# Optimization experiments

Hardware: AMD Instinct MI355X
Metric: run time of the kernel (lower is better)

Reference implementation:

```python
import jax, jax.numpy as jnp
from jax import lax
import numpy as np

NUM_CLASSES = 10
NUM_ITERS = 3


def conv2d(x, w, stride):
    return lax.conv_general_dilated(x, w, window_strides=stride, padding='VALID',
                                    dimension_numbers=('NCHW', 'OIHW', 'NCHW'))


def deconv(x, w_torch, stride, pad):
    # w_torch: [Cin, Cout, k, k] (PyTorch ConvTranspose2d layout)
    k = w_torch.shape[2]
    w = jnp.flip(w_torch, axis=(2, 3)).transpose(1, 0, 2, 3)  # -> [Cout, Cin, k, k]
    return lax.conv_general_dilated(x, w, window_strides=(1, 1),
                                    padding=[(k - 1 - pad, k - 1 - pad)] * 2,
                                    lhs_dilation=(stride, stride),
                                    dimension_numbers=('NCHW', 'OIHW', 'NCHW'))


def squash(t, axis=-1):
    sq = jnp.sum(t * t, axis=axis, keepdims=True)
    return (sq / (1.0 + sq)) * t / jnp.sqrt(sq)


def batchnorm(t, g, b, eps=1e-5):
    # training-mode batch statistics over (N, H, W)
    m = t.mean(axis=(0, 2, 3), keepdims=True)
    v = t.var(axis=(0, 2, 3), keepdims=True)
    return g[None, :, None, None] * (t - m) / jnp.sqrt(v + eps) + b[None, :, None, None]


def setup_inputs() -> dict:
    key = jax.random.key(0)
    ks = jax.random.split(key, 16)
    B = 128
    d = dict(
        x=jax.random.normal(ks[0], (B, 3, 32, 32), jnp.float32),
        conv1_w=jax.random.normal(ks[1], (256, 3, 9, 9), jnp.float32) * 0.05,
        conv1_b=jnp.zeros((256,), jnp.float32),
        prim_w=jax.random.normal(ks[2], (8, 64, 256, 9, 9), jnp.float32) * 0.02,
        prim_b=jnp.zeros((8, 64), jnp.float32),
        route_w=jax.random.normal(ks[3], (NUM_CLASSES, 4096, 8, 16), jnp.float32),
        g1_w=jax.random.normal(ks[4], (160, 256, 4, 4), jnp.float32) * 0.02,
        g2_w=jax.random.normal(ks[5], (256, 128, 4, 4), jnp.float32) * 0.02,
        g3_w=jax.random.normal(ks[6], (128, 64, 4, 4), jnp.float32) * 0.02,
        g4_w=jax.random.normal(ks[7], (64, 3, 4, 4), jnp.float32) * 0.02,
        bn1_g=jnp.ones((256,), jnp.float32), bn1_b=jnp.zeros((256,), jnp.float32),
        bn2_g=jnp.ones((128,), jnp.float32), bn2_b=jnp.zeros((128,), jnp.float32),
        bn3_g=jnp.ones((64,), jnp.float32), bn3_b=jnp.zeros((64,), jnp.float32),
    )
    return d


def reference(x, conv1_w, conv1_b, prim_w, prim_b, route_w,
              g1_w, g2_w, g3_w, g4_w,
              bn1_g, bn1_b, bn2_g, bn2_b, bn3_g, bn3_b):
    B = x.shape[0]
    # conv stem: [B,3,32,32] -> [B,256,24,24]
    h = jax.nn.relu(conv2d(x, conv1_w, (1, 1)) + conv1_b[None, :, None, None])
    # primary capsules: 8 parallel convs fused into one [8*64,256,9,9] conv -> [B,512,8,8]
    u = conv2d(h, prim_w.reshape(8 * 64, 256, 9, 9), (2, 2)) + prim_b.reshape(8 * 64)[None, :, None, None]
    # cat over capsules on last dim: route node = flat (c,h,w) per capsule -> [B,4096,8]
    u = u.reshape(B, 8, 64 * 8 * 8).transpose(0, 2, 1)
    u = squash(u, axis=-1)
    # digit capsules: priors [C,B,R,16]
    priors = jnp.einsum('bri,crio->cbro', u, route_w)
    logits = jnp.zeros(priors.shape[:3], priors.dtype)  # [C,B,R]
    v = None
    for i in range(NUM_ITERS):
        probs = jax.nn.softmax(logits, axis=2)  # over route nodes (dim=2 in original)
        v = squash(jnp.einsum('cbr,cbro->cbo', probs, priors), axis=-1)  # [C,B,16]
        if i != NUM_ITERS - 1:
            logits = logits + jnp.einsum('cbro,cbo->cbr', priors, v)
    caps = v.transpose(1, 0, 2)  # [B,10,16]
    classes = jax.nn.softmax(jnp.sqrt(jnp.sum(caps * caps, axis=-1)), axis=-1)  # [B,10]
    # y = one-hot of predicted class (inference path, y=None)
    y = jax.nn.one_hot(jnp.argmax(classes, axis=1), NUM_CLASSES, dtype=caps.dtype)
    z = (caps * y[:, :, None]).reshape(B, 160, 1, 1)
    # DCGAN generator: 1 -> 4 -> 8 -> 16 -> 32
    t = jax.nn.relu(batchnorm(deconv(z, g1_w, 1, 0), bn1_g, bn1_b))
    t = jax.nn.relu(batchnorm(deconv(t, g2_w, 2, 1), bn2_g, bn2_b))
    t = jax.nn.relu(batchnorm(deconv(t, g3_w, 2, 1), bn3_g, bn3_b))
    recon = jnp.tanh(deconv(t, g4_w, 2, 1))  # [B,3,32,32]
    return classes, recon
```

## Files before the change

### kernel.cpp

```cpp
#include <hip/hip_runtime.h>
#include <cmath>

#define NB 128

#define H_STRIDE 600
#define W_SLAB   7776

__global__ __launch_bounds__(192) void conv1_kernel(
    const float* __restrict__ x, const float* __restrict__ w,
    const float* __restrict__ bias, float* __restrict__ h)
{
    __shared__ float4 xs4[768];
    float* xs = (float*)xs4;
    int b = blockIdx.x, cobase = blockIdx.y * 8, tid = threadIdx.x;
    const float4* xsrc = (const float4*)(x + (size_t)b * 3072);
    for (int i = tid; i < 768; i += 192) xs4[i] = xsrc[i];
    __syncthreads();
    for (int round = 0; round < 3; ++round) {
        int px = round * 192 + tid;
        int yy = px / 24, xx = px - yy * 24;
        float acc[8];
        #pragma unroll
        for (int cc = 0; cc < 8; ++cc) acc[cc] = 0.f;
        for (int c = 0; c < 3; ++c)
            for (int ky = 0; ky < 9; ++ky) {
                const float* xr = xs + c * 1024 + (yy + ky) * 32 + xx;
                float xv[9];
                #pragma unroll
                for (int kx = 0; kx < 9; ++kx) xv[kx] = xr[kx];
                int tb = c * 81 + ky * 9;
                #pragma unroll
                for (int cc = 0; cc < 8; ++cc) {
                    const float* wp = w + (cobase + cc) * 243 + tb;
                    #pragma unroll
                    for (int kx = 0; kx < 9; ++kx) acc[cc] += xv[kx] * wp[kx];
                }
            }
        #pragma unroll
        for (int cc = 0; cc < 8; ++cc)
            h[((size_t)b * 256 + cobase + cc) * H_STRIDE + yy * 25 + xx] =
                fmaxf(acc[cc] + bias[cobase + cc], 0.f);
    }
}

__global__ __launch_bounds__(128) void primw_transpose_kernel(
    const float* __restrict__ pw, float* __restrict__ wt)
{
    int g = blockIdx.x >> 8, ci = blockIdx.x & 255;
    int half = threadIdx.x >> 6, lane = threadIdx.x & 63;
    for (int ch = half; ch < 64; ch += 2) {
        int oct = ch >> 3, k = ch & 7;
        const float* src = pw + ((size_t)(g * 64 + ch) * 256 + ci) * 81;
        float* dst = wt + (size_t)(g * 256 + ci) * W_SLAB + oct * 12 + k;
        dst[(size_t)lane * 96] = src[lane];
        if (lane < 17) dst[(size_t)(64 + lane) * 96] = src[64 + lane];
    }
}

__global__ __launch_bounds__(128) void prim_conv_kernel(
    const float* __restrict__ h, const float* __restrict__ wt,
    float* __restrict__ part)
{
    __shared__ __align__(16) float wsh[W_SLAB];
    __shared__ __align__(16) float hsh[H_STRIDE];
    int b = blockIdx.x, g = blockIdx.y, half = blockIdx.z, tid = threadIdx.x;
    int ci0 = half * 128;
    int oct = tid & 7;
    int pq = tid >> 3;
    int px0 = pq * 4;
    int y0 = pq >> 1, x0 = (pq & 1) * 4;

    float acc[8][4];
    #pragma unroll
    for (int i = 0; i < 8; ++i)
        #pragma unroll
        for (int j = 0; j < 4; ++j) acc[i][j] = 0.f;

    #define STAGE(ci)                                                                        \
    {                                                                                        \
        const float* wsrc = wt + (size_t)(g * 256 + (ci)) * W_SLAB;                          \
        const float* hsrc = h + ((size_t)b * 256 + (ci)) * H_STRIDE;                         \
        _Pragma("unroll")                                                                    \
        for (int k = 0; k < 16; ++k) {                                                       \
            int ix = k * 128 + tid;                                                          \
            if (ix < 1944)                                                                   \
                __builtin_amdgcn_global_load_lds(                                            \
                    (const unsigned int*)wsrc + ix * 4,                                      \
                    (unsigned int*)wsh + ix * 4, 16, 0, 0);                                  \
        }                                                                                    \
        __builtin_amdgcn_global_load_lds(                                                    \
            (const unsigned int*)hsrc + tid * 4,                                             \
            (unsigned int*)hsh + tid * 4, 16, 0, 0);                                         \
        if (tid < 22)                                                                        \
            __builtin_amdgcn_global_load_lds(                                                \
                (const unsigned int*)hsrc + (128 + tid) * 4,                                 \
                (unsigned int*)hsh + (128 + tid) * 4, 16, 0, 0);                             \
    }

    STAGE(ci0);
    asm volatile("s_waitcnt vmcnt(0)" ::: "memory");
    __syncthreads();

    for (int ci = ci0; ci < ci0 + 128; ++ci) {
        #pragma unroll 3
        for (int ky = 0; ky < 9; ++ky) {
            int hrowbase = (2 * y0 + ky) * 25 + 2 * x0;
            #pragma unroll
            for (int kx = 0; kx < 9; ++kx) {
                const float* wp = wsh + (ky * 9 + kx) * 96 + oct * 12;
                float4 wa = *(const float4*)(wp);
                float4 wb = *(const float4*)(wp + 4);
                int hr = hrowbase + kx;
                float h0 = hsh[hr];
                float h1 = hsh[hr + 2];
                float h2 = hsh[hr + 4];
                float h3 = hsh[hr + 6];
                float wv[8] = {wa.x, wa.y, wa.z, wa.w, wb.x, wb.y, wb.z, wb.w};
                #pragma unroll
                for (int i = 0; i < 8; ++i) {
                    acc[i][0] += wv[i] * h0;
                    acc[i][1] += wv[i] * h1;
                    acc[i][2] += wv[i] * h2;
                    acc[i][3] += wv[i] * h3;
                }
            }
        }
        __syncthreads();
        if (ci + 1 < ci0 + 128) STAGE(ci + 1);
        asm volatile("s_waitcnt vmcnt(0)" ::: "memory");
        __syncthreads();
    }
    #undef STAGE

    float* pp = part + ((size_t)(half * 128 + b) * 8 + g) * 4096;
    #pragma unroll
    for (int i = 0; i < 8; ++i) {
        int c64 = oct * 8 + i;
        *(float4*)(pp + c64 * 64 + px0) =
            make_float4(acc[i][0], acc[i][1], acc[i][2], acc[i][3]);
    }
}

__global__ void squash_u_kernel(const float* __restrict__ part,
                                const float* __restrict__ pb, float* __restrict__ ut)
{
    int b = blockIdx.x; int r = blockIdx.y * 256 + threadIdx.x;
    int c64 = r >> 6;
    const float* p0 = part + (size_t)b * 8 * 4096 + r;
    const float* p1 = part + (size_t)(128 + b) * 8 * 4096 + r;
    float v[8]; float sq = 0.f;
    #pragma unroll
    for (int i = 0; i < 8; ++i) {
        v[i] = p0[(size_t)i * 4096] + p1[(size_t)i * 4096] + pb[i * 64 + c64];
        sq += v[i] * v[i];
    }
    float sc = sqrtf(sq) / (1.f + sq);
    float4 o0 = make_float4(v[0] * sc, v[1] * sc, v[2] * sc, v[3] * sc);
    float4 o1 = make_float4(v[4] * sc, v[5] * sc, v[6] * sc, v[7] * sc);
    float* o = ut + ((size_t)b * 4096 + r) * 8;
    *(float4*)o = o0; *(float4*)(o + 4) = o1;
}

__global__ void softmax_stats_kernel(const float* __restrict__ logits,
                                     float* __restrict__ mbuf, float* __restrict__ sebuf)
{
    int cb = blockIdx.x; int tid = threadIdx.x;
    const float* lrow = logits + (size_t)cb * 4096;
    float mx = -1e30f;
    for (int i = tid; i < 4096; i += 256) mx = fmaxf(mx, lrow[i]);
    #pragma unroll
    for (int d = 1; d < 64; d <<= 1) mx = fmaxf(mx, __shfl_xor(mx, d));
    __shared__ float rm[4], rs[4];
    if ((tid & 63) == 0) rm[tid >> 6] = mx;
    __syncthreads();
    mx = fmaxf(fmaxf(rm[0], rm[1]), fmaxf(rm[2], rm[3]));
    float s = 0.f;
    for (int i = tid; i < 4096; i += 256) s += expf(lrow[i] - mx);
    #pragma unroll
    for (int d = 1; d < 64; d <<= 1) s += __shfl_xor(s, d);
    if ((tid & 63) == 0) rs[tid >> 6] = s;
    __syncthreads();
    if (tid == 0) {
        mbuf[cb] = mx;
        sebuf[cb] = rs[0] + rs[1] + rs[2] + rs[3];
    }
}

__global__ __launch_bounds__(256) void route_s_kernel(
    const float* __restrict__ logits, const float* __restrict__ ut,
    const float* __restrict__ route_w, const float* __restrict__ mbuf,
    const float* __restrict__ sebuf, float* __restrict__ spart)
{
    __shared__ __align__(16) float smem[11232];
    const int UB = 4224, PB = 8400, RB = 8928;
    int c = blockIdx.x, ch = blockIdx.y, tid = threadIdx.x;
    int r0 = ch * 32;

    {
        const float4* w4 = (const float4*)(route_w + ((size_t)c * 4096 + r0) * 128);
        #pragma unroll
        for (int k = 0; k < 4; ++k) {
            int idx = k * 256 + tid;
            float4 wv = w4[idx];
            int rl = idx >> 5, rem = (idx & 31) * 4;
            *(float4*)(smem + rl * 132 + rem) = wv;
        }
    }

    int bC = tid & 15, igC = (tid >> 4) & 7, ohC = tid >> 7;

    for (int bg = 0; bg < 8; ++bg) {
        int b0 = bg * 16;
        __syncthreads();
        {
            int bb = tid >> 4, seg = tid & 15;
            const float4* us = (const float4*)(ut + (size_t)(b0 + bb) * 32768 + (size_t)r0 * 8);
            #pragma unroll
            for (int q = 0; q < 4; ++q) {
                float4 v = us[seg * 4 + q];
                int base = UB + bb * 261 + (seg * 4 + q) * 4;
                smem[base + 0] = v.x; smem[base + 1] = v.y;
                smem[base + 2] = v.z; smem[base + 3] = v.w;
            }
        }
        if (tid < 128) {
            int b = tid >> 3, rr = tid & 7;
            int cb = c * 128 + b0 + b;
            float m = mbuf[cb];
            float inv = 1.0f / sebuf[cb];
            float4 lv = *(const float4*)(logits + (size_t)cb * 4096 + r0 + rr * 4);
            int pbb = PB + b * 33 + rr * 4;
            smem[pbb + 0] = expf(lv.x - m) * inv;
            smem[pbb + 1] = expf(lv.y - m) * inv;
            smem[pbb + 2] = expf(lv.z - m) * inv;
            smem[pbb + 3] = expf(lv.w - m) * inv;
        }
        __syncthreads();
        float4 a0 = make_float4(0.f, 0.f, 0.f, 0.f);
        float4 a1 = make_float4(0.f, 0.f, 0.f, 0.f);
        int ub = UB + bC * 261 + igC;
        int wb = igC * 16 + ohC * 8;
        int pbb = PB + bC * 33;
        for (int rl = 0; rl < 32; ++rl) {
            float uu = smem[ub + rl * 8];
            float pr = smem[pbb + rl];
            float t1 = pr * uu;
            const float* wp = smem + rl * 132 + wb;
            float4 w0 = *(const float4*)wp;
            float4 w1 = *(const float4*)(wp + 4);
            a0.x += t1 * w0.x; a0.y += t1 * w0.y; a0.z += t1 * w0.z; a0.w += t1 * w0.w;
            a1.x += t1 * w1.x; a1.y += t1 * w1.y; a1.z += t1 * w1.z; a1.w += t1 * w1.w;
        }
        int rb = RB + tid * 9;
        smem[rb + 0] = a0.x; smem[rb + 1] = a0.y; smem[rb + 2] = a0.z; smem[rb + 3] = a0.w;
        smem[rb + 4] = a1.x; smem[rb + 5] = a1.y; smem[rb + 6] = a1.z; smem[rb + 7] = a1.w;
        __syncthreads();
        {
            int o = tid & 15, b = tid >> 4;
            int oh = o >> 3, ol = o & 7;
            float s = 0.f;
            #pragma unroll
            for (int ig = 0; ig < 8; ++ig)
                s += smem[RB + (b + 16 * ig + 128 * oh) * 9 + ol];
            spart[(size_t)ch * 20480 + (size_t)(c * 128 + b0 + b) * 16 + o] = s;
        }
    }
}

__global__ void route_v_kernel(const float* __restrict__ spart, float* __restrict__ vbuf)
{
    int cb = blockIdx.x * 64 + threadIdx.x;
    float4 a0 = make_float4(0,0,0,0), a1 = make_float4(0,0,0,0);
    float4 a2 = make_float4(0,0,0,0), a3 = make_float4(0,0,0,0);
    for (int k = 0; k < 128; ++k) {
        const float4* p = (const float4*)(spart + (size_t)k * 20480 + (size_t)cb * 16);
        float4 b0 = p[0], b1 = p[1], b2 = p[2], b3 = p[3];
        a0.x += b0.x; a0.y += b0.y; a0.z += b0.z; a0.w += b0.w;
        a1.x += b1.x; a1.y += b1.y; a1.z += b1.z; a1.w += b1.w;
        a2.x += b2.x; a2.y += b2.y; a2.z += b2.z; a2.w += b2.w;
        a3.x += b3.x; a3.y += b3.y; a3.z += b3.z; a3.w += b3.w;
    }
    float sq = a0.x*a0.x + a0.y*a0.y + a0.z*a0.z + a0.w*a0.w
             + a1.x*a1.x + a1.y*a1.y + a1.z*a1.z + a1.w*a1.w
             + a2.x*a2.x + a2.y*a2.y + a2.z*a2.z + a2.w*a2.w
             + a3.x*a3.x + a3.y*a3.y + a3.z*a3.z + a3.w*a3.w;
    float sc = sqrtf(sq) / (1.f + sq);
    float4* vp = (float4*)(vbuf + (size_t)cb * 16);
    vp[0] = make_float4(a0.x*sc, a0.y*sc, a0.z*sc, a0.w*sc);
    vp[1] = make_float4(a1.x*sc, a1.y*sc, a1.z*sc, a1.w*sc);
    vp[2] = make_float4(a2.x*sc, a2.y*sc, a2.z*sc, a2.w*sc);
    vp[3] = make_float4(a3.x*sc, a3.y*sc, a3.z*sc, a3.w*sc);
}

__global__ __launch_bounds__(256) void route_upd_kernel(
    float* __restrict__ logits, const float* __restrict__ ut,
    const float* __restrict__ route_w, const float* __restrict__ vbuf)
{
    __shared__ __align__(16) float smem[8400];
    const int UB = 4224;
    int c = blockIdx.x, ch = blockIdx.y, tid = threadIdx.x;
    int r0 = ch * 32;
    {
        const float4* w4 = (const float4*)(route_w + ((size_t)c * 4096 + r0) * 128);
        #pragma unroll
        for (int k = 0; k < 4; ++k) {
            int idx = k * 256 + tid;
            float4 wv = w4[idx];
            int rl = idx >> 5, rem = (idx & 31) * 4;
            *(float4*)(smem + rl * 132 + rem) = wv;
        }
    }
    int b = tid & 15, rg = tid >> 4;
    for (int bg = 0; bg < 8; ++bg) {
        int b0 = bg * 16;
        __syncthreads();
        {
            int bb = tid >> 4, seg = tid & 15;
            const float4* us = (const float4*)(ut + (size_t)(b0 + bb) * 32768 + (size_t)r0 * 8);
            #pragma unroll
            for (int q = 0; q < 4; ++q) {
                float4 v = us[seg * 4 + q];
                int base = UB + bb * 261 + (seg * 4 + q) * 4;
                smem[base + 0] = v.x; smem[base + 1] = v.y;
                smem[base + 2] = v.z; smem[base + 3] = v.w;
            }
        }
        __syncthreads();
        int cb = c * 128 + b0 + b;
        const float4* vp = (const float4*)(vbuf + (size_t)cb * 16);
        float4 v0 = vp[0], v1 = vp[1], v2 = vp[2], v3 = vp[3];
        #pragma unroll
        for (int jj = 0; jj < 2; ++jj) {
            int rl = rg * 2 + jj;
            float4 p0 = make_float4(0,0,0,0), p1 = make_float4(0,0,0,0);
            float4 p2 = make_float4(0,0,0,0), p3 = make_float4(0,0,0,0);
            int ub = UB + b * 261 + rl * 8;
            #pragma unroll
            for (int i = 0; i < 8; ++i) {
                float uu = smem[ub + i];
                const float* wp = smem + rl * 132 + i * 16;
                float4 w0 = *(const float4*)wp;
                float4 w1 = *(const float4*)(wp + 4);
                float4 w2 = *(const float4*)(wp + 8);
                float4 w3 = *(const float4*)(wp + 12);
                p0.x += uu*w0.x; p0.y += uu*w0.y; p0.z += uu*w0.z; p0.w += uu*w0.w;
                p1.x += uu*w1.x; p1.y += uu*w1.y; p1.z += uu*w1.z; p1.w += uu*w1.w;
                p2.x += uu*w2.x; p2.y += uu*w2.y; p2.z += uu*w2.z; p2.w += uu*w2.w;
                p3.x += uu*w3.x; p3.y += uu*w3.y; p3.z += uu*w3.z; p3.w += uu*w3.w;
            }
            float delta = p0.x*v0.x + p0.y*v0.y + p0.z*v0.z + p0.w*v0.w
                        + p1.x*v1.x + p1.y*v1.y + p1.z*v1.z + p1.w*v1.w
                        + p2.x*v2.x + p2.y*v2.y + p2.z*v2.z + p2.w*v2.w
                        + p3.x*v3.x + p3.y*v3.y + p3.z*v3.z + p3.w*v3.w;
            logits[(size_t)cb * 4096 + r0 + rl] += delta;
        }
    }
}

__global__ void caps_out_kernel(const float* __restrict__ vbuf,
                                float* __restrict__ out_classes, float* __restrict__ zbuf)
{
    int b = threadIdx.x;
    float norms[10];
    #pragma unroll
    for (int c = 0; c < 10; ++c) {
        const float* vp = vbuf + (size_t)(c * 128 + b) * 16;
        float sq = 0.f;
        #pragma unroll
        for (int o = 0; o < 16; ++o) sq += vp[o] * vp[o];
        norms[c] = sqrtf(sq);
    }
    float mx = norms[0]; int am = 0;
    #pragma unroll
    for (int c = 1; c < 10; ++c) if (norms[c] > mx) { mx = norms[c]; am = c; }
    float se = 0.f; float e[10];
    #pragma unroll
    for (int c = 0; c < 10; ++c) { e[c] = expf(norms[c] - mx); se += e[c]; }
    float isd = 1.f / se;
    #pragma unroll
    for (int c = 0; c < 10; ++c) out_classes[b * 10 + c] = e[c] * isd;
    #pragma unroll
    for (int c = 0; c < 10; ++c) {
        const float* vp = vbuf + (size_t)(c * 128 + b) * 16;
        #pragma unroll
        for (int o = 0; o < 16; ++o)
            zbuf[b * 160 + c * 16 + o] = (c == am) ? vp[o] : 0.f;
    }
}

__global__ void gen1_kernel(const float* __restrict__ z, const float* __restrict__ w,
                            float* __restrict__ out)
{
    int idx = blockIdx.x * 256 + threadIdx.x;
    int j = idx & 4095; int b = idx >> 12;
    const float* zp = z + b * 160;
    float a = 0.f;
    #pragma unroll 4
    for (int ci = 0; ci < 160; ++ci) a += zp[ci] * w[(size_t)ci * 4096 + j];
    out[idx] = a;
}

template <int C, int HW>
__global__ void bn_stats_kernel(const float* __restrict__ t, const float* __restrict__ g,
                                const float* __restrict__ beta,
                                float* __restrict__ scale, float* __restrict__ shift)
{
    int co = blockIdx.x; int tid = threadIdx.x;
    float s = 0.f, s2 = 0.f;
    for (int i = tid; i < NB * HW; i += 256) {
        int b = i / HW, hw = i - b * HW;
        float v = t[((size_t)b * C + co) * HW + hw];
        s += v; s2 += v * v;
    }
    #pragma unroll
    for (int d = 1; d < 64; d <<= 1) { s += __shfl_xor(s, d); s2 += __shfl_xor(s2, d); }
    __shared__ float rs[4], rs2[4];
    if ((tid & 63) == 0) { rs[tid >> 6] = s; rs2[tid >> 6] = s2; }
    __syncthreads();
    if (tid == 0) {
        float S = rs[0] + rs[1] + rs[2] + rs[3];
        float S2 = rs2[0] + rs2[1] + rs2[2] + rs2[3];
        const float n = (float)(NB * HW);
        float mean = S / n;
        float var = S2 / n - mean * mean;
        float r = 1.f / sqrtf(var + 1e-5f);
        scale[co] = g[co] * r;
        shift[co] = beta[co] - mean * g[co] * r;
    }
}

template <int C, int HW>
__global__ void bn_apply_kernel(float* __restrict__ t, const float* __restrict__ scale,
                                const float* __restrict__ shift, int total)
{
    int idx = blockIdx.x * 256 + threadIdx.x;
    if (idx < total) {
        int co = (idx / HW) % C;
        t[idx] = fmaxf(t[idx] * scale[co] + shift[co], 0.f);
    }
}

template <int Ci, int Co, int S, int SPLIT>
__global__ __launch_bounds__(256) void deconv_row_kernel(
    const float* __restrict__ in, const float* __restrict__ w,
    float* __restrict__ out)
{
    constexpr int OS = 2 * S;
    constexpr int ROWS = Co * OS;
    constexpr int RPB = ROWS / SPLIT;
    __shared__ __align__(16) float ish[Ci * S * S];
    int b = blockIdx.x, rb = blockIdx.y, tid = threadIdx.x;
    const float4* src = (const float4*)(in + (size_t)b * Ci * S * S);
    for (int i = tid; i < Ci * S * S / 4; i += 256) ((float4*)ish)[i] = src[i];
    __syncthreads();

    for (int r = rb * RPB + tid; r < (rb + 1) * RPB; r += 256) {
        int co = r / OS, oy = r % OS;
        float acc[OS];
        #pragma unroll
        for (int j = 0; j < OS; ++j) acc[j] = 0.f;
        int p = (oy + 1) & 1;
        for (int ci = 0; ci < Ci; ++ci) {
            const float* wci = w + ((size_t)ci * Co + co) * 16;
            #pragma unroll
            for (int t = 0; t < 2; ++t) {
                int ky = p + 2 * t;
                int iy = (oy + 1 - ky) >> 1;
                if (iy < 0 || iy >= S) continue;
                float4 wv = *(const float4*)(wci + ky * 4);
                const float* irow = ish + (ci * S + iy) * S;
                #pragma unroll
                for (int ox = 0; ox < OS; ++ox) {
                    constexpr int dummy = 0; (void)dummy;
                    int q = (ox + 1) & 1;
                    int ix0 = (ox + 1 - q) >> 1;
                    int ix1 = ix0 - 1;
                    float wk0 = q ? wv.y : wv.x;
                    float wk2 = q ? wv.w : wv.z;
                    if (ix0 < S)  acc[ox] += wk0 * irow[ix0];
                    if (ix1 >= 0) acc[ox] += wk2 * irow[ix1];
                }
            }
        }
        float* orow = out + ((size_t)(b * Co + co) * OS + oy) * OS;
        #pragma unroll
        for (int j = 0; j < OS; j += 4)
            *(float4*)(orow + j) = make_float4(acc[j], acc[j+1], acc[j+2], acc[j+3]);
    }
}

template <int Ci, int Co, int S, bool TANH>
__global__ void deconv_kernel(const float* __restrict__ in, const float* __restrict__ w,
                              float* __restrict__ out)
{
    constexpr int OS = 2 * S;
    int idx = blockIdx.x * 256 + threadIdx.x;
    int ox = idx % OS; int t = idx / OS;
    int oy = t % OS; int t2 = t / OS;
    int co = t2 % Co; int b = t2 / Co;
    float a = 0.f;
    #pragma unroll
    for (int ky = 0; ky < 4; ++ky) {
        int ty = oy + 1 - ky;
        if (ty & 1) continue;
        int iy = ty >> 1;
        if (iy < 0 || iy >= S) continue;
        #pragma unroll
        for (int kx = 0; kx < 4; ++kx) {
            int tx = ox + 1 - kx;
            if (tx & 1) continue;
            int ix = tx >> 1;
            if (ix < 0 || ix >= S) continue;
            const float* ip = in + ((size_t)b * Ci * S + iy) * S + ix;
            const float* wp = w + co * 16 + ky * 4 + kx;
            #pragma unroll 4
            for (int ci = 0; ci < Ci; ++ci)
                a += ip[(size_t)ci * S * S] * wp[(size_t)ci * Co * 16];
        }
    }
    out[idx] = TANH ? tanhf(a) : a;
}

extern "C" void kernel_launch(void* const* d_in, const int* in_sizes, int n_in,
                              void* d_out, int out_size, void* d_ws, size_t ws_size,
                              hipStream_t stream)
{
    const float* x       = (const float*)d_in[0];
    const float* conv1_w = (const float*)d_in[1];
    const float* conv1_b = (const float*)d_in[2];
    const float* prim_w  = (const float*)d_in[3];
    const float* prim_b  = (const float*)d_in[4];
    const float* route_w = (const float*)d_in[5];
    const float* g1_w    = (const float*)d_in[6];
    const float* g2_w    = (const float*)d_in[7];
    const float* g3_w    = (const float*)d_in[8];
    const float* g4_w    = (const float*)d_in[9];
    const float* bn1_g   = (const float*)d_in[10];
    const float* bn1_b   = (const float*)d_in[11];
    const float* bn2_g   = (const float*)d_in[12];
    const float* bn2_b   = (const float*)d_in[13];
    const float* bn3_g   = (const float*)d_in[14];
    const float* bn3_b   = (const float*)d_in[15];
    float* outf = (float*)d_out;

    float* ws = (float*)d_ws;
    float* h      = ws;
    float* wt     = h + 19660800;
    float* part   = wt + 15925248;
    float* logits = wt;
    float* ut     = wt + 5242880;
    float* mbuf   = part;
    float* sebuf  = part + 1280;
    float* vbuf   = part + 2560;
    float* zbuf   = part + 23040;
    float* bnsc   = part + 64000;
    float* t1b    = part + 64896;
    float* t2b    = part + 589184;
    float* t3b    = part + 1637760;
    float* spart  = part + 4194304;

    primw_transpose_kernel<<<dim3(2048), 128, 0, stream>>>(prim_w, wt);
    conv1_kernel<<<dim3(128, 32), 192, 0, stream>>>(x, conv1_w, conv1_b, h);
    prim_conv_kernel<<<dim3(128, 8, 2), 128, 0, stream>>>(h, wt, part);
    squash_u_kernel<<<dim3(128, 16), 256, 0, stream>>>(part, prim_b, ut);

    hipMemsetAsync(logits, 0, (size_t)5242880 * sizeof(float), stream);
    for (int it = 0; it < 3; ++it) {
        softmax_stats_kernel<<<dim3(1280), 256, 0, stream>>>(logits, mbuf, sebuf);
        route_s_kernel<<<dim3(10, 128), 256, 0, stream>>>(logits, ut, route_w, mbuf, sebuf, spart);
        route_v_kernel<<<dim3(20), 64, 0, stream>>>(spart, vbuf);
        if (it < 2)
            route_upd_kernel<<<dim3(10, 128), 256, 0, stream>>>(logits, ut, route_w, vbuf);
    }
    caps_out_kernel<<<dim3(1), 128, 0, stream>>>(vbuf, outf, zbuf);

    gen1_kernel<<<dim3(2048), 256, 0, stream>>>(zbuf, g1_w, t1b);
    bn_stats_kernel<256, 16><<<dim3(256), 256, 0, stream>>>(t1b, bn1_g, bn1_b, bnsc, bnsc + 256);
    bn_apply_kernel<256, 16><<<dim3(2048), 256, 0, stream>>>(t1b, bnsc, bnsc + 256, 524288);

    deconv_row_kernel<256, 128, 4, 4><<<dim3(128, 4), 256, 0, stream>>>(t1b, g2_w, t2b);
    bn_stats_kernel<128, 64><<<dim3(128), 256, 0, stream>>>(t2b, bn2_g, bn2_b, bnsc + 512, bnsc + 640);
    bn_apply_kernel<128, 64><<<dim3(4096), 256, 0, stream>>>(t2b, bnsc + 512, bnsc + 640, 1048576);

    deconv_row_kernel<128, 64, 8, 4><<<dim3(128, 4), 256, 0, stream>>>(t2b, g3_w, t3b);
    bn_stats_kernel<64, 256><<<dim3(64), 256, 0, stream>>>(t3b, bn3_g, bn3_b, bnsc + 768, bnsc + 832);
    bn_apply_kernel<64, 256><<<dim3(8192), 256, 0, stream>>>(t3b, bnsc + 768, bnsc + 832, 2097152);

    deconv_kernel<64, 3, 16, true><<<dim3(1536), 256, 0, stream>>>(t3b, g4_w, outf + 1280);
}
```

Before: 4.441 ms.

## Process two images per prim_conv block to share weight slab staging

Each prim_conv block now handles two batch images with 256 threads, staging one weight slab per input channel into LDS and reusing it for both images. This halves the global-to-LDS weight traffic per output and the number of blocks, at the cost of twice the LDS for activations and fewer blocks in the grid. The unused constexpr in the deconv loop is dropped as cleanup.

```diff
diff --git a/kernel.cpp b/kernel.cpp
--- a/kernel.cpp
+++ b/kernel.cpp
@@ -57,18 +57,22 @@
     }
 }
 
-__global__ __launch_bounds__(128) void prim_conv_kernel(
+__global__ __launch_bounds__(256) void prim_conv_kernel(
     const float* __restrict__ h, const float* __restrict__ wt,
     float* __restrict__ part)
 {
     __shared__ __align__(16) float wsh[W_SLAB];
-    __shared__ __align__(16) float hsh[H_STRIDE];
-    int b = blockIdx.x, g = blockIdx.y, half = blockIdx.z, tid = threadIdx.x;
+    __shared__ __align__(16) float hsh[2 * H_STRIDE];
+    int b2 = blockIdx.x, g = blockIdx.y, half = blockIdx.z, tid = threadIdx.x;
     int ci0 = half * 128;
-    int oct = tid & 7;
-    int pq = tid >> 3;
+    int img = tid >> 7;
+    int t128 = tid & 127;
+    int oct = t128 & 7;
+    int pq = t128 >> 3;
     int px0 = pq * 4;
     int y0 = pq >> 1, x0 = (pq & 1) * 4;
+    int b = b2 * 2 + img;
+    int hbase = img * H_STRIDE;
 
     float acc[8][4];
     #pragma unroll
@@ -79,22 +83,25 @@
     #define STAGE(ci)                                                                        \
     {                                                                                        \
         const float* wsrc = wt + (size_t)(g * 256 + (ci)) * W_SLAB;                          \
-        const float* hsrc = h + ((size_t)b * 256 + (ci)) * H_STRIDE;                         \
+        const float* h0src = h + ((size_t)(b2 * 2 + 0) * 256 + (ci)) * H_STRIDE;             \
+        const float* h1src = h + ((size_t)(b2 * 2 + 1) * 256 + (ci)) * H_STRIDE;             \
         _Pragma("unroll")                                                                    \
-        for (int k = 0; k < 16; ++k) {                                                       \
-            int ix = k * 128 + tid;                                                          \
-            if (ix < 1944)                                                                   \
-                __builtin_amdgcn_global_load_lds(                                            \
-                    (const unsigned int*)wsrc + ix * 4,                                      \
-                    (unsigned int*)wsh + ix * 4, 16, 0, 0);                                  \
-        }                                                                                    \
-        __builtin_amdgcn_global_load_lds(                                                    \
-            (const unsigned int*)hsrc + tid * 4,                                             \
-            (unsigned int*)hsh + tid * 4, 16, 0, 0);                                         \
-        if (tid < 22)                                                                        \
+        for (int k = 0; k < 7; ++k)                                                          \
             __builtin_amdgcn_global_load_lds(                                                \
-                (const unsigned int*)hsrc + (128 + tid) * 4,                                 \
-                (unsigned int*)hsh + (128 + tid) * 4, 16, 0, 0);                             \
+                (const unsigned int*)wsrc + (k * 256 + tid) * 4,                             \
+                (unsigned int*)wsh + (k * 256 + tid) * 4, 16, 0, 0);                         \
+        if (tid < 152)                                                                       \
+            __builtin_amdgcn_global_load_lds(                                                \
+                (const unsigned int*)wsrc + (1792 + tid) * 4,                                \
+                (unsigned int*)wsh + (1792 + tid) * 4, 16, 0, 0);                            \
+        if (tid < 150)                                                                       \
+            __builtin_amdgcn_global_load_lds(                                                \
+                (const unsigned int*)h0src + tid * 4,                                        \
+                (unsigned int*)hsh + tid * 4, 16, 0, 0);                                     \
+        if (tid < 150)                                                                       \
+            __builtin_amdgcn_global_load_lds(                                                \
+                (const unsigned int*)h1src + tid * 4,                                        \
+                (unsigned int*)(hsh + H_STRIDE) + tid * 4, 16, 0, 0);                        \
     }
 
     STAGE(ci0);
@@ -104,7 +111,7 @@
     for (int ci = ci0; ci < ci0 + 128; ++ci) {
         #pragma unroll 3
         for (int ky = 0; ky < 9; ++ky) {
-            int hrowbase = (2 * y0 + ky) * 25 + 2 * x0;
+            int hrowbase = hbase + (2 * y0 + ky) * 25 + 2 * x0;
             #pragma unroll
             for (int kx = 0; kx < 9; ++kx) {
                 const float* wp = wsh + (ky * 9 + kx) * 96 + oct * 12;
@@ -471,7 +478,6 @@
                 const float* irow = ish + (ci * S + iy) * S;
                 #pragma unroll
                 for (int ox = 0; ox < OS; ++ox) {
-                    constexpr int dummy = 0; (void)dummy;
                     int q = (ox + 1) & 1;
                     int ix0 = (ox + 1 - q) >> 1;
                     int ix1 = ix0 - 1;
@@ -561,7 +567,7 @@
 
     primw_transpose_kernel<<<dim3(2048), 128, 0, stream>>>(prim_w, wt);
     conv1_kernel<<<dim3(128, 32), 192, 0, stream>>>(x, conv1_w, conv1_b, h);
-    prim_conv_kernel<<<dim3(128, 8, 2), 128, 0, stream>>>(h, wt, part);
+    prim_conv_kernel<<<dim3(64, 8, 2), 256, 0, stream>>>(h, wt, part);
     squash_u_kernel<<<dim3(128, 16), 256, 0, stream>>>(part, prim_b, ut);
 
     hipMemsetAsync(logits, 0, (size_t)5242880 * sizeof(float), stream);
```

After: 4.031 ms. 1.1x faster.
